# Kernel optimization log

Measured on AMD Instinct MI355X. Metric: run time of the kernel, lower is better.

## Reference

```python
import jax, jax.numpy as jnp
import numpy as np

B = 16384
IN = 1024      # 2*input_dim
H = 1024       # hidden_dim
K = IN + H     # gate input size


def setup_inputs() -> dict:
    key = jax.random.key(0)
    ks = jax.random.split(key, 20)
    x = jax.random.normal(ks[0], (B, IN), dtype=jnp.float32)
    n_id = jax.random.randint(ks[1], (B,), 0, 16384, dtype=jnp.int64) if jax.config.jax_enable_x64 else jax.random.randint(ks[1], (B,), 0, 16384).astype(jnp.int32)
    t = jax.random.uniform(ks[2], (B,), dtype=jnp.float32)
    last_t = jnp.zeros((B,), dtype=jnp.float32)
    s = 1.0 / np.sqrt(K)
    def lin(k):
        k1, k2 = jax.random.split(k)
        W = jax.random.uniform(k1, (K, H), minval=-s, maxval=s, dtype=jnp.float32)
        b = jax.random.uniform(k2, (H,), minval=-s, maxval=s, dtype=jnp.float32)
        return W, b
    Wi, bi = lin(ks[3])
    Wit, bit = lin(ks[4])
    Wf, bf = lin(ks[5])
    Wft, bft = lin(ks[6])
    Wz, bz = lin(ks[7])
    Wo, bo = lin(ks[8])
    Wd, bd = lin(ks[9])
    return dict(x=x, n_id=n_id, t=t, last_t=last_t,
                Wi=Wi, bi=bi, Wit=Wit, bit=bit, Wf=Wf, bf=bf,
                Wft=Wft, bft=bft, Wz=Wz, bz=bz, Wo=Wo, bo=bo, Wd=Wd, bd=bd)


def reference(x, n_id, t, last_t, Wi, bi, Wit, bit, Wf, bf, Wft, bft, Wz, bz, Wo, bo, Wd, bd):
    batch = x.shape[0]
    h = jnp.zeros((batch, H), dtype=x.dtype)
    c = jnp.zeros((batch, H), dtype=x.dtype)
    c_target = jnp.zeros((batch, H), dtype=x.dtype)

    k = jnp.concatenate([x, h], axis=1)  # [B, K]
    # fuse 7 gate GEMMs into one: [B,K] @ [K,7H]
    W = jnp.concatenate([Wi, Wit, Wf, Wft, Wz, Wo, Wd], axis=1)
    b = jnp.concatenate([bi, bit, bf, bft, bz, bo, bd])
    g = k @ W + b  # [B, 7H]
    gi, git, gf, gft, gz, go, gd = jnp.split(g, 7, axis=1)

    gate_i = jax.nn.sigmoid(gi)
    gate_i_target = jax.nn.sigmoid(git)
    gate_f = jax.nn.sigmoid(gf)
    gate_f_target = jax.nn.sigmoid(gft)
    gate_o = jax.nn.sigmoid(go)
    z = 2.0 * jax.nn.sigmoid(gz) - 1.0
    c_n = gate_f * c + gate_i * z
    c_target_n = gate_f_target * c_target + gate_i_target * z
    delta = jax.nn.softplus(gd)

    delta_t = (t - last_t)[:, None]  # [B,1]
    cell = c_target_n + (c_n - c_target_n) * jnp.exp(-delta * delta_t)
    h_n = gate_o * jnp.tanh(cell)
    return (h_n, c_n, c_target_n, gate_o, delta)
```

## Files before the change

### kernel.cpp

```cpp
#include <hip/hip_runtime.h>


#define B_SZ 16384
#define H_SZ 1024
#define K_SZ 1024
#define BH ((size_t)B_SZ * H_SZ)
#define NGATE 5
#define CHUNK 512
#define BUFU (28 * CHUNK)

typedef __bf16 bf16x8 __attribute__((ext_vector_type(8)));
typedef float f32x4 __attribute__((ext_vector_type(4)));

__device__ __forceinline__ unsigned short f2bf(float f) {
    unsigned int u = __float_as_uint(f);
    u += 0x7FFFu + ((u >> 16) & 1u);
    return (unsigned short)(u >> 16);
}

__device__ __forceinline__ float rcp_fast(float x) { return __builtin_amdgcn_rcpf(x); }
__device__ __forceinline__ float sigm(float x) { return rcp_fast(1.f + __expf(-x)); }
__device__ __forceinline__ float softplus_f(float x) {
    return fmaxf(x, 0.f) + __logf(1.f + __expf(-fabsf(x)));
}
__device__ __forceinline__ float tanh_f(float x) {
    float e = __expf(2.f * x);
    return (e - 1.f) * rcp_fast(e + 1.f);
}

__global__ void conv_x_kernel(const float* __restrict__ x, unsigned short* __restrict__ xb) {
    int i = blockIdx.x * blockDim.x + threadIdx.x;
    float4 v = ((const float4*)x)[i];
    ushort4 o;
    o.x = f2bf(v.x); o.y = f2bf(v.y); o.z = f2bf(v.z); o.w = f2bf(v.w);
    ((ushort4*)xb)[i] = o;
}

__global__ void conv_w_kernel(const float* __restrict__ W0, const float* __restrict__ W1,
                              const float* __restrict__ W2, const float* __restrict__ W3,
                              const float* __restrict__ W4, unsigned short* __restrict__ wt) {
    const float* Ws[NGATE] = {W0, W1, W2, W3, W4};
    const float* W = Ws[blockIdx.z];
    __shared__ float tile[64][65];
    const int k0 = blockIdx.x * 64, n0 = blockIdx.y * 64;
    const int tid = threadIdx.x;
    {
        const int kk = tid >> 6, nn = tid & 63;
#pragma unroll
        for (int rr = 0; rr < 16; rr++) {
            const int row = kk * 16 + rr;
            tile[row][nn] = W[(size_t)(k0 + row) * H_SZ + n0 + nn];
        }
    }
    __syncthreads();
    unsigned short* out = wt + (size_t)blockIdx.z * H_SZ * K_SZ;
    {
        const int nrow = tid >> 2, kq = (tid & 3) * 16;
#pragma unroll
        for (int j = 0; j < 4; j++) {
            const int k = kq + j * 4;
            ushort4 v;
            v.x = f2bf(tile[k + 0][nrow]);
            v.y = f2bf(tile[k + 1][nrow]);
            v.z = f2bf(tile[k + 2][nrow]);
            v.w = f2bf(tile[k + 3][nrow]);
            *(ushort4*)&out[(size_t)(n0 + nrow) * K_SZ + k0 + k] = v;
        }
    }
}

__global__ __launch_bounds__(256, 2) void fused_clstm_kernel(
    const unsigned short* __restrict__ xb,
    const unsigned short* __restrict__ wt,
    const float* __restrict__ bi, const float* __restrict__ bit_,
    const float* __restrict__ bz, const float* __restrict__ bo,
    const float* __restrict__ bd,
    const float* __restrict__ t, const float* __restrict__ last_t,
    float* __restrict__ out)
{
    __shared__ unsigned short smem[2 * BUFU];

    const int tid  = threadIdx.x;
    const int wave = tid >> 6;
    const int lane = tid & 63;
    const int quad = lane >> 4;
    const int l16  = lane & 15;
    const int wm   = wave >> 1;
    const int wn   = wave & 1;

    const int s     = blockIdx.y * 16 + blockIdx.x;
    const int xcd   = s & 7;
    const int jj    = s >> 3;
    const int n_blk = xcd * 2 + (jj >> 7);
    const int m_blk = jj & 127;
    const int m0    = m_blk * 128;
    const int n0    = n_blk * 64;

    const int srow = lane >> 2;
    const int scol = ((lane & 3) ^ (srow & 3)) * 8;
    const int xq   = (quad ^ (l16 & 3)) * 8;

    const unsigned short* gbase[7];
#pragma unroll
    for (int i = 0; i < 7; i++) {
        const int c = wave * 7 + i;
        if (c < 8) {
            gbase[i] = xb + (size_t)(m0 + c * 16 + srow) * K_SZ + scol;
        } else {
            const int g = (c - 8) >> 2, q = (c - 8) & 3;
            gbase[i] = wt + (size_t)g * H_SZ * K_SZ
                          + (size_t)(n0 + q * 16 + srow) * K_SZ + scol;
        }
    }

    f32x4 acc[NGATE][4][2];
#pragma unroll
    for (int g = 0; g < NGATE; g++)
#pragma unroll
        for (int mf = 0; mf < 4; mf++)
#pragma unroll
            for (int nf = 0; nf < 2; nf++)
                acc[g][mf][nf] = (f32x4){0.f, 0.f, 0.f, 0.f};

#define STAGE(bufi, kk) do {                                                          \
    _Pragma("unroll")                                                                 \
    for (int i = 0; i < 7; i++) {                                                     \
        __builtin_amdgcn_global_load_lds(                                             \
            (const __attribute__((address_space(1))) unsigned int*)(gbase[i] + (kk)), \
            (__attribute__((address_space(3))) unsigned int*)                         \
                (&smem[(bufi) * BUFU + (wave * 7 + i) * CHUNK + lane * 8]),           \
            16, 0, 0);                                                                \
    } } while (0)

#define COMPUTE(bufi) do {                                                            \
    const unsigned short* sb_ = &smem[(bufi) * BUFU];                                 \
    bf16x8 a_[4];                                                                     \
    _Pragma("unroll")                                                                 \
    for (int mf = 0; mf < 4; mf++)                                                    \
        a_[mf] = *(const bf16x8*)(&sb_[(wm * 64 + mf * 16 + l16) * 32 + xq]);         \
    __builtin_amdgcn_s_setprio(1);                                                    \
    _Pragma("unroll")                                                                 \
    for (int g = 0; g < NGATE; g++) {                                                 \
        const unsigned short* bs_ = &sb_[(8 + g * 4) * CHUNK];                        \
        const bf16x8 b0 = *(const bf16x8*)(&bs_[(wn * 32      + l16) * 32 + xq]);     \
        const bf16x8 b1 = *(const bf16x8*)(&bs_[(wn * 32 + 16 + l16) * 32 + xq]);     \
        _Pragma("unroll")                                                             \
        for (int mf = 0; mf < 4; mf++) {                                              \
            acc[g][mf][0] = __builtin_amdgcn_mfma_f32_16x16x32_bf16(a_[mf], b0, acc[g][mf][0], 0, 0, 0); \
            acc[g][mf][1] = __builtin_amdgcn_mfma_f32_16x16x32_bf16(a_[mf], b1, acc[g][mf][1], 0, 0, 0); \
        } }                                                                           \
    __builtin_amdgcn_s_setprio(0); } while (0)

    STAGE(0, 0);
    __syncthreads();

#pragma unroll 1
    for (int k0 = 0; k0 < K_SZ - 64; k0 += 64) {
        STAGE(1, k0 + 32);
        __builtin_amdgcn_sched_barrier(0);
        COMPUTE(0);
        __syncthreads();
        STAGE(0, k0 + 64);
        __builtin_amdgcn_sched_barrier(0);
        COMPUTE(1);
        __syncthreads();
    }
    STAGE(1, K_SZ - 32);
    __builtin_amdgcn_sched_barrier(0);
    COMPUTE(0);
    __syncthreads();
    COMPUTE(1);
#undef STAGE
#undef COMPUTE

    const float* biasp[NGATE] = {bi, bit_, bz, bo, bd};
    float bv[NGATE][2];
#pragma unroll
    for (int g = 0; g < NGATE; g++)
#pragma unroll
        for (int nf = 0; nf < 2; nf++)
            bv[g][nf] = biasp[g][n0 + wn * 32 + nf * 16 + l16];

#pragma unroll
    for (int mf = 0; mf < 4; mf++) {
#pragma unroll
        for (int r = 0; r < 4; r++) {
            const int brow = m0 + wm * 64 + mf * 16 + quad * 4 + r;
            const float dt = t[brow] - last_t[brow];
#pragma unroll
            for (int nf = 0; nf < 2; nf++) {
                const int ncol = n0 + wn * 32 + nf * 16 + l16;
                const float gi  = acc[0][mf][nf][r] + bv[0][nf];
                const float git = acc[1][mf][nf][r] + bv[1][nf];
                const float gz  = acc[2][mf][nf][r] + bv[2][nf];
                const float go  = acc[3][mf][nf][r] + bv[3][nf];
                const float gd  = acc[4][mf][nf][r] + bv[4][nf];

                const float gate_i  = sigm(gi);
                const float gate_it = sigm(git);
                const float z       = 2.f * sigm(gz) - 1.f;
                const float gate_o  = sigm(go);
                const float delta   = softplus_f(gd);

                const float c_n  = gate_i  * z;
                const float ct_n = gate_it * z;
                const float cell = ct_n + (c_n - ct_n) * __expf(-delta * dt);
                const float h_n  = gate_o * tanh_f(cell);

                const size_t idx = (size_t)brow * H_SZ + ncol;
                __builtin_nontemporal_store(h_n,    &out[idx]);
                __builtin_nontemporal_store(c_n,    &out[BH + idx]);
                __builtin_nontemporal_store(ct_n,   &out[2 * BH + idx]);
                __builtin_nontemporal_store(gate_o, &out[3 * BH + idx]);
                __builtin_nontemporal_store(delta,  &out[4 * BH + idx]);
            }
        }
    }
}

extern "C" void kernel_launch(void* const* d_in, const int* in_sizes, int n_in,
                              void* d_out, int out_size, void* d_ws, size_t ws_size,
                              hipStream_t stream) {
    const float* x      = (const float*)d_in[0];
    const float* t      = (const float*)d_in[2];
    const float* last_t = (const float*)d_in[3];
    const float* Wi  = (const float*)d_in[4];
    const float* bi  = (const float*)d_in[5];
    const float* Wit = (const float*)d_in[6];
    const float* bit_= (const float*)d_in[7];
    const float* Wz  = (const float*)d_in[12];
    const float* bz  = (const float*)d_in[13];
    const float* Wo  = (const float*)d_in[14];
    const float* bo  = (const float*)d_in[15];
    const float* Wd  = (const float*)d_in[16];
    const float* bd  = (const float*)d_in[17];

    unsigned short* xb = (unsigned short*)d_ws;
    unsigned short* wt = xb + (size_t)B_SZ * K_SZ;

    conv_x_kernel<<<(B_SZ * K_SZ / 4) / 256, 256, 0, stream>>>(x, xb);

    dim3 gw(16, 16, NGATE);
    conv_w_kernel<<<gw, 256, 0, stream>>>(Wi, Wit, Wz, Wo, Wd, wt);

    dim3 gm(H_SZ / 64, B_SZ / 128);
    fused_clstm_kernel<<<gm, 256, 0, stream>>>(xb, wt, bi, bit_, bz, bo, bd,
                                               t, last_t, (float*)d_out);
}
```

Measured before the change: 622.3 us.

## Load A operand directly into registers, drop LDS swizzle and XCD block remap

Each wave now loads its A (activation) fragments straight from global memory into registers with double-buffered register sets, and only the B weight tiles go through LDS via global_load_lds. This shrinks the LDS buffer from 28 to 20 chunks. The XOR bank swizzle on LDS reads is removed, the XCD-aware block index remapping is replaced by plain blockIdx mapping, and the nontemporal output stores become ordinary stores. The A tile is duplicated across the two wn waves (redundant global loads), and dropping the swizzle may reintroduce LDS bank conflicts and hurt L2 locality.

```diff
diff --git a/kernel.cpp b/kernel.cpp
--- a/kernel.cpp
+++ b/kernel.cpp
@@ -7,7 +7,8 @@
 #define BH ((size_t)B_SZ * H_SZ)
 #define NGATE 5
 #define CHUNK 512
-#define BUFU (28 * CHUNK)
+#define NCHUNK 20
+#define BUFU (NCHUNK * CHUNK)
 
 typedef __bf16 bf16x8 __attribute__((ext_vector_type(8)));
 typedef float f32x4 __attribute__((ext_vector_type(4)));
@@ -87,30 +88,24 @@
     const int l16  = lane & 15;
     const int wm   = wave >> 1;
     const int wn   = wave & 1;
-
-    const int s     = blockIdx.y * 16 + blockIdx.x;
-    const int xcd   = s & 7;
-    const int jj    = s >> 3;
-    const int n_blk = xcd * 2 + (jj >> 7);
-    const int m_blk = jj & 127;
-    const int m0    = m_blk * 128;
-    const int n0    = n_blk * 64;
+    const int m0   = blockIdx.y * 128;
+    const int n0   = blockIdx.x * 64;
 
     const int srow = lane >> 2;
-    const int scol = ((lane & 3) ^ (srow & 3)) * 8;
-    const int xq   = (quad ^ (l16 & 3)) * 8;
-
-    const unsigned short* gbase[7];
-#pragma unroll
-    for (int i = 0; i < 7; i++) {
-        const int c = wave * 7 + i;
-        if (c < 8) {
-            gbase[i] = xb + (size_t)(m0 + c * 16 + srow) * K_SZ + scol;
-        } else {
-            const int g = (c - 8) >> 2, q = (c - 8) & 3;
-            gbase[i] = wt + (size_t)g * H_SZ * K_SZ
-                          + (size_t)(n0 + q * 16 + srow) * K_SZ + scol;
-        }
+    const int scol = (lane & 3) * 8;
+
+    const unsigned short* aBase[4];
+#pragma unroll
+    for (int mf = 0; mf < 4; mf++)
+        aBase[mf] = xb + (size_t)(m0 + wm * 64 + mf * 16 + l16) * K_SZ + quad * 8;
+
+    const unsigned short* gbase[5];
+#pragma unroll
+    for (int i = 0; i < 5; i++) {
+        const int c = wave * 5 + i;
+        const int g = c >> 2, q = c & 3;
+        gbase[i] = wt + (size_t)g * H_SZ * K_SZ
+                      + (size_t)(n0 + q * 16 + srow) * K_SZ + scol;
     }
 
     f32x4 acc[NGATE][4][2];
@@ -122,55 +117,64 @@
             for (int nf = 0; nf < 2; nf++)
                 acc[g][mf][nf] = (f32x4){0.f, 0.f, 0.f, 0.f};
 
-#define STAGE(bufi, kk) do {                                                          \
+    bf16x8 aP[4], aQ[4];
+
+#define LOADA(dst, kk) do {                                                           \
     _Pragma("unroll")                                                                 \
-    for (int i = 0; i < 7; i++) {                                                     \
+    for (int mf = 0; mf < 4; mf++)                                                    \
+        dst[mf] = *(const bf16x8*)(aBase[mf] + (kk));                                 \
+    } while (0)
+
+#define STAGE_B(bufi, kk) do {                                                        \
+    _Pragma("unroll")                                                                 \
+    for (int i = 0; i < 5; i++) {                                                     \
         __builtin_amdgcn_global_load_lds(                                             \
             (const __attribute__((address_space(1))) unsigned int*)(gbase[i] + (kk)), \
             (__attribute__((address_space(3))) unsigned int*)                         \
-                (&smem[(bufi) * BUFU + (wave * 7 + i) * CHUNK + lane * 8]),           \
+                (&smem[(bufi) * BUFU + (wave * 5 + i) * CHUNK + lane * 8]),           \
             16, 0, 0);                                                                \
     } } while (0)
 
-#define COMPUTE(bufi) do {                                                            \
+#define COMPUTE(bufi, aReg) do {                                                      \
     const unsigned short* sb_ = &smem[(bufi) * BUFU];                                 \
-    bf16x8 a_[4];                                                                     \
-    _Pragma("unroll")                                                                 \
-    for (int mf = 0; mf < 4; mf++)                                                    \
-        a_[mf] = *(const bf16x8*)(&sb_[(wm * 64 + mf * 16 + l16) * 32 + xq]);         \
     __builtin_amdgcn_s_setprio(1);                                                    \
     _Pragma("unroll")                                                                 \
     for (int g = 0; g < NGATE; g++) {                                                 \
-        const unsigned short* bs_ = &sb_[(8 + g * 4) * CHUNK];                        \
-        const bf16x8 b0 = *(const bf16x8*)(&bs_[(wn * 32      + l16) * 32 + xq]);     \
-        const bf16x8 b1 = *(const bf16x8*)(&bs_[(wn * 32 + 16 + l16) * 32 + xq]);     \
+        const unsigned short* bs_ = &sb_[(g * 4) * CHUNK];                            \
+        const bf16x8 b0 = *(const bf16x8*)(&bs_[(wn * 32      + l16) * 32 + quad * 8]); \
+        const bf16x8 b1 = *(const bf16x8*)(&bs_[(wn * 32 + 16 + l16) * 32 + quad * 8]); \
         _Pragma("unroll")                                                             \
         for (int mf = 0; mf < 4; mf++) {                                              \
-            acc[g][mf][0] = __builtin_amdgcn_mfma_f32_16x16x32_bf16(a_[mf], b0, acc[g][mf][0], 0, 0, 0); \
-            acc[g][mf][1] = __builtin_amdgcn_mfma_f32_16x16x32_bf16(a_[mf], b1, acc[g][mf][1], 0, 0, 0); \
+            acc[g][mf][0] = __builtin_amdgcn_mfma_f32_16x16x32_bf16(aReg[mf], b0, acc[g][mf][0], 0, 0, 0); \
+            acc[g][mf][1] = __builtin_amdgcn_mfma_f32_16x16x32_bf16(aReg[mf], b1, acc[g][mf][1], 0, 0, 0); \
         } }                                                                           \
     __builtin_amdgcn_s_setprio(0); } while (0)
 
-    STAGE(0, 0);
+    LOADA(aP, 0);
+    STAGE_B(0, 0);
     __syncthreads();
 
 #pragma unroll 1
     for (int k0 = 0; k0 < K_SZ - 64; k0 += 64) {
-        STAGE(1, k0 + 32);
+        LOADA(aQ, k0 + 32);
+        STAGE_B(1, k0 + 32);
         __builtin_amdgcn_sched_barrier(0);
-        COMPUTE(0);
+        COMPUTE(0, aP);
         __syncthreads();
-        STAGE(0, k0 + 64);
+        LOADA(aP, k0 + 64);
+        STAGE_B(0, k0 + 64);
         __builtin_amdgcn_sched_barrier(0);
-        COMPUTE(1);
+        COMPUTE(1, aQ);
         __syncthreads();
     }
-    STAGE(1, K_SZ - 32);
+    LOADA(aQ, K_SZ - 32);
+    STAGE_B(1, K_SZ - 32);
     __builtin_amdgcn_sched_barrier(0);
-    COMPUTE(0);
+    COMPUTE(0, aP);
     __syncthreads();
-    COMPUTE(1);
-#undef STAGE
+    COMPUTE(1, aQ);
+#undef LOADA
+#undef STAGE_B
 #undef COMPUTE
 
     const float* biasp[NGATE] = {bi, bit_, bz, bo, bd};
@@ -208,11 +212,11 @@
                 const float h_n  = gate_o * tanh_f(cell);
 
                 const size_t idx = (size_t)brow * H_SZ + ncol;
-                __builtin_nontemporal_store(h_n,    &out[idx]);
-                __builtin_nontemporal_store(c_n,    &out[BH + idx]);
-                __builtin_nontemporal_store(ct_n,   &out[2 * BH + idx]);
-                __builtin_nontemporal_store(gate_o, &out[3 * BH + idx]);
-                __builtin_nontemporal_store(delta,  &out[4 * BH + idx]);
+                out[idx]          = h_n;
+                out[BH + idx]     = c_n;
+                out[2 * BH + idx] = ct_n;
+                out[3 * BH + idx] = gate_o;
+                out[4 * BH + idx] = delta;
             }
         }
     }
```

After: 630.4 us. Within noise of the previous version (+1.3%).
